# Kernel tuning notes

Hardware: AMD Instinct MI355X
Metric: run time of the kernel (lower is better)

Reference implementation:

```python
import jax, jax.numpy as jnp
import numpy as np

N = 24000; E = 384000; NT = 3; IN = 128; HID = 32; ED = 64; NE = 5; FFN = 64; C = 16
HEADS = (8, 8, 1); ALPHA = 0.05; DAL = 2


def _lrelu(x, s):
    return jnp.where(x >= 0, x, s * x)


def _elu(x):
    return jnp.where(x > 0, x, jnp.expm1(x))


def _ln(x, g, b, eps=1e-5):
    m = x.mean(-1, keepdims=True)
    v = ((x - m) ** 2).mean(-1, keepdims=True)
    return (x - m) / jnp.sqrt(v + eps) * g + b


def _l2n(x, eps=1e-12):
    return x / jnp.maximum(jnp.linalg.norm(x, axis=1, keepdims=True), eps)


def _ta(h, src, dst, e_feat, edge_emb, W, We, al, ar, ae, bias, res_W, res_attn, act):
    # SimpleHGN-style heterogeneous graph attention layer (TALayer)
    Hh = al.shape[0]
    feat = (h @ W).reshape(N, Hh, HID)                       # [N,H,D]
    ee = (edge_emb[e_feat] @ We).reshape(E, Hh, ED)          # [E,H,ED]
    el = (feat * al).sum(-1)                                 # [N,H]
    er = (feat * ar).sum(-1)                                 # [N,H]
    lg = _lrelu(el[src] + er[dst] + (ee * ae).sum(-1), 0.2)  # [E,H]
    m = jax.ops.segment_max(lg, dst, num_segments=N)         # edge softmax over dst
    a = jnp.exp(lg - m[dst])
    a = a / jax.ops.segment_sum(a, dst, num_segments=N)[dst]
    if res_attn is not None:
        a = a * (1.0 - ALPHA) + res_attn * ALPHA             # residual attention carry-over
    rst = jax.ops.segment_sum(a[:, :, None] * feat[src], dst, num_segments=N)
    if res_W is not None:
        rst = rst + (h @ res_W).reshape(N, Hh, HID)
    rst = rst + bias
    if act:
        rst = _elu(rst)
    return rst, jax.lax.stop_gradient(a)


def forward(feats, fc_W, fc_b, ntype_emb, W_ntype,
            ta0_edge_emb, ta0_W, ta0_We, ta0_al, ta0_ar, ta0_ae, ta0_bias,
            ta1_edge_emb, ta1_W, ta1_We, ta1_al, ta1_ar, ta1_ae, ta1_bias, ta1_res_W,
            ta2_edge_emb, ta2_W, ta2_We, ta2_al, ta2_ar, ta2_ae, ta2_bias, ta2_res_W,
            da_ln1_g, da_ln1_b, da_Wq, da_bq, da_Wk, da_bk, da_Wv, da_bv, da_Wo, da_bo,
            da_ln2_g, da_ln2_b, da_W1, da_b1, da_W2, da_b2, final_W, logits_W,
            e_feat, node_type, src, dst):
    # per-node-type input projection + leaky_relu(0.01), concat over types -> [N,HID]
    h = _lrelu(jnp.einsum('tni,tio->tno', feats, fc_W) + fc_b[:, None, :], 0.01).reshape(N, HID)
    ntype_feat = (ntype_emb @ W_ntype)[node_type]            # [N,HID]
    h = h * ntype_feat
    h0, a0 = _ta(h, src, dst, e_feat, ta0_edge_emb, ta0_W, ta0_We, ta0_al, ta0_ar, ta0_ae, ta0_bias, None, None, True)
    h = h0.reshape(N, -1)
    h1, _ = _ta(h, src, dst, e_feat, ta1_edge_emb, ta1_W, ta1_We, ta1_al, ta1_ar, ta1_ae, ta1_bias, ta1_res_W, a0, True)
    h = h1.reshape(N, -1)
    hf, _ = _ta(h, src, dst, e_feat, ta2_edge_emb, ta2_W, ta2_We, ta2_al, ta2_ar, ta2_ae, ta2_bias, ta2_res_W, None, False)
    h_feat = hf.reshape(N, HID)
    # dim-wise transformer (DALayer stack): tokens = HID dims, channel = 1
    x = (h_feat * ntype_feat)[:, :, None]                    # [N,HID,1]
    for l in range(DAL):
        y = _ln(x, da_ln1_g[l], da_ln1_b[l])
        q = y @ da_Wq[l] + da_bq[l]
        k = y @ da_Wk[l] + da_bk[l]
        v = y @ da_Wv[l] + da_bv[l]
        att = jax.nn.softmax(jnp.einsum('nqd,nkd->nqk', q, k), axis=-1)  # scale=att_size**-0.5=1
        x = x + (jnp.einsum('nqk,nkd->nqd', att, v) @ da_Wo[l] + da_bo[l])
        y = _ln(x, da_ln2_g[l], da_ln2_b[l])
        x = x + (jax.nn.gelu(y @ da_W1[l] + da_b1[l], approximate=False) @ da_W2[l] + da_b2[l])
    h_dim = _l2n(x[:, :, 0])
    h_final = jnp.concatenate([_l2n(h_feat), h_dim], axis=1) @ final_W
    logits = jax.nn.relu(h_final) @ logits_W
    return logits / jnp.maximum(jnp.linalg.norm(logits, axis=1, keepdims=True), 1e-12)


def setup_inputs():
    key = jax.random.key(0)
    ks = iter(jax.random.split(key, 96))
    def rn(shape, s=0.1):
        return jax.random.normal(next(ks), shape, jnp.float32) * s
    inp = {}
    inp["feats"] = jax.random.normal(next(ks), (NT, N // NT, IN), jnp.float32)
    inp["e_feat"] = jax.random.randint(next(ks), (E,), 0, NE)
    inp["node_type"] = jax.random.randint(next(ks), (N,), 0, NT)
    inp["src"] = jax.random.randint(next(ks), (E,), 0, N)
    inp["dst"] = jax.random.randint(next(ks), (E,), 0, N)
    inp["fc_W"] = rn((NT, IN, HID)); inp["fc_b"] = rn((NT, HID))
    inp["ntype_emb"] = rn((NT, HID)); inp["W_ntype"] = rn((HID, HID))
    ins = (HID, HID * HEADS[0], HID * HEADS[1])
    for l in range(3):
        Hh = HEADS[l]; di = ins[l]; p = "ta%d_" % l
        inp[p + "edge_emb"] = rn((NE, ED))
        inp[p + "W"] = rn((di, Hh * HID))
        inp[p + "We"] = rn((ED, Hh * ED))
        inp[p + "al"] = rn((Hh, HID)); inp[p + "ar"] = rn((Hh, HID)); inp[p + "ae"] = rn((Hh, ED))
        inp[p + "bias"] = jnp.zeros((Hh, HID), jnp.float32)
        if l > 0:
            inp[p + "res_W"] = rn((di, Hh * HID))
    inp["da_ln1_g"] = jnp.ones((DAL, 1), jnp.float32); inp["da_ln1_b"] = jnp.zeros((DAL, 1), jnp.float32)
    inp["da_Wq"] = rn((DAL, 1, 1)); inp["da_bq"] = jnp.zeros((DAL, 1), jnp.float32)
    inp["da_Wk"] = rn((DAL, 1, 1)); inp["da_bk"] = jnp.zeros((DAL, 1), jnp.float32)
    inp["da_Wv"] = rn((DAL, 1, 1)); inp["da_bv"] = jnp.zeros((DAL, 1), jnp.float32)
    inp["da_Wo"] = rn((DAL, 1, 1)); inp["da_bo"] = jnp.zeros((DAL, 1), jnp.float32)
    inp["da_ln2_g"] = jnp.ones((DAL, 1), jnp.float32); inp["da_ln2_b"] = jnp.zeros((DAL, 1), jnp.float32)
    inp["da_W1"] = rn((DAL, 1, FFN)); inp["da_b1"] = jnp.zeros((DAL, FFN), jnp.float32)
    inp["da_W2"] = rn((DAL, FFN, 1)); inp["da_b2"] = jnp.zeros((DAL, 1), jnp.float32)
    inp["final_W"] = rn((2 * HID, HID))
    inp["logits_W"] = rn((HID, C))
    return inp


def reference(feats, fc_W, fc_b, ntype_emb, W_ntype,
              ta0_edge_emb, ta0_W, ta0_We, ta0_al, ta0_ar, ta0_ae, ta0_bias,
              ta1_edge_emb, ta1_W, ta1_We, ta1_al, ta1_ar, ta1_ae, ta1_bias, ta1_res_W,
              ta2_edge_emb, ta2_W, ta2_We, ta2_al, ta2_ar, ta2_ae, ta2_bias, ta2_res_W,
              da_ln1_g, da_ln1_b, da_Wq, da_bq, da_Wk, da_bk, da_Wv, da_bv, da_Wo, da_bo,
              da_ln2_g, da_ln2_b, da_W1, da_b1, da_W2, da_b2, final_W, logits_W,
              e_feat, node_type, src, dst):
    return forward(feats, fc_W, fc_b, ntype_emb, W_ntype,
                   ta0_edge_emb, ta0_W, ta0_We, ta0_al, ta0_ar, ta0_ae, ta0_bias,
                   ta1_edge_emb, ta1_W, ta1_We, ta1_al, ta1_ar, ta1_ae, ta1_bias, ta1_res_W,
                   ta2_edge_emb, ta2_W, ta2_We, ta2_al, ta2_ar, ta2_ae, ta2_bias, ta2_res_W,
                   da_ln1_g, da_ln1_b, da_Wq, da_bq, da_Wk, da_bk, da_Wv, da_bv, da_Wo, da_bo,
                   da_ln2_g, da_ln2_b, da_W1, da_b1, da_W2, da_b2, final_W, logits_W,
                   e_feat, node_type, src, dst)
```

## Files before the change

### kernel.cpp

```cpp
#include <hip/hip_runtime.h>
#include <math.h>

constexpr int kN = 24000;
constexpr int kE = 384000;
constexpr float kAlpha = 0.05f;

typedef unsigned int   u32;
typedef unsigned short u16;
typedef __attribute__((ext_vector_type(8))) short short8;
typedef __attribute__((ext_vector_type(4))) float float4v;

__device__ __forceinline__ float bf2f(u16 x) { return __uint_as_float(((u32)x) << 16); }
__device__ __forceinline__ u16 f2bf(float f) {
  u32 u = __float_as_uint(f);
  return (u16)((u + 0x7fffu + ((u >> 16) & 1u)) >> 16);
}
__device__ __forceinline__ void bfrow32(const u16* __restrict__ p, float* f) {
  const uint4* q = (const uint4*)p;
  #pragma unroll
  for (int i = 0; i < 4; ++i) {
    uint4 w = q[i];
    f[i*8+0] = bf2f((u16)(w.x & 0xffff)); f[i*8+1] = bf2f((u16)(w.x >> 16));
    f[i*8+2] = bf2f((u16)(w.y & 0xffff)); f[i*8+3] = bf2f((u16)(w.y >> 16));
    f[i*8+4] = bf2f((u16)(w.z & 0xffff)); f[i*8+5] = bf2f((u16)(w.z >> 16));
    f[i*8+6] = bf2f((u16)(w.w & 0xffff)); f[i*8+7] = bf2f((u16)(w.w >> 16));
  }
}

__global__ void __launch_bounds__(256) zero_ints_kernel(int* __restrict__ p, int n) {
  int i = blockIdx.x * 256 + threadIdx.x;
  if (i < n) p[i] = 0;
}

__global__ void __launch_bounds__(256) count_kernel(const int* __restrict__ dst,
                                                    int* __restrict__ counts) {
  int e = blockIdx.x * 256 + threadIdx.x;
  if (e < kE) atomicAdd(&counts[dst[e]], 1);
}

__global__ void __launch_bounds__(1024) scan_kernel(const int* __restrict__ counts,
                                                    int* __restrict__ row_start) {
  __shared__ int wsum[16];
  __shared__ int carry_s;
  int tid = threadIdx.x, lane = tid & 63, wid = tid >> 6;
  if (tid == 0) { carry_s = 0; row_start[0] = 0; }
  __syncthreads();
  for (int base = 0; base < kN; base += 1024) {
    int x = (base + tid < kN) ? counts[base + tid] : 0;
    #pragma unroll
    for (int off = 1; off < 64; off <<= 1) {
      int y = __shfl_up(x, off);
      if (lane >= off) x += y;
    }
    if (lane == 63) wsum[wid] = x;
    __syncthreads();
    if (tid < 16) {
      int wv = wsum[tid];
      #pragma unroll
      for (int off = 1; off < 16; off <<= 1) {
        int y = __shfl_up(wv, off);
        if (tid >= off) wv += y;
      }
      wsum[tid] = wv;
    }
    __syncthreads();
    int incl = x + carry_s + (wid > 0 ? wsum[wid - 1] : 0);
    if (base + tid < kN) row_start[base + tid + 1] = incl;
    __syncthreads();
    if (tid == 1023) carry_s = incl;
    __syncthreads();
  }
}

__global__ void __launch_bounds__(256) scatter_kernel(const int* __restrict__ dst,
                                                      const int* __restrict__ row_start,
                                                      int* __restrict__ cursor,
                                                      int* __restrict__ edge_ids) {
  int e = blockIdx.x * 256 + threadIdx.x;
  if (e < kE) {
    int n = dst[e];
    int pos = row_start[n] + atomicAdd(&cursor[n], 1);
    edge_ids[pos] = e;
  }
}

__global__ void __launch_bounds__(1024) precompute_kernel(
    const float* __restrict__ ntype_emb, const float* __restrict__ W_ntype,
    const float* __restrict__ emb0, const float* __restrict__ We0, const float* __restrict__ ae0,
    const float* __restrict__ emb1, const float* __restrict__ We1, const float* __restrict__ ae1,
    const float* __restrict__ emb2, const float* __restrict__ We2, const float* __restrict__ ae2,
    const float* __restrict__ ln1_b, const float* __restrict__ Wv, const float* __restrict__ bv,
    const float* __restrict__ Wo, const float* __restrict__ bo,
    const float* __restrict__ ln2_b, const float* __restrict__ W1, const float* __restrict__ b1,
    const float* __restrict__ W2, const float* __restrict__ b2,
    float* __restrict__ ntf, float* __restrict__ eterm, float* __restrict__ dadelta) {
  __shared__ float wae[17][64];
  __shared__ float red[128];
  int tid = threadIdx.x;
  for (int idx = tid; idx < 17 * 64; idx += 1024) {
    int hg = idx >> 6, k = idx & 63;
    const float* We; const float* ae; int Hh, h;
    if (hg < 8)       { We = We0; ae = ae0; Hh = 8; h = hg; }
    else if (hg < 16) { We = We1; ae = ae1; Hh = 8; h = hg - 8; }
    else              { We = We2; ae = ae2; Hh = 1; h = 0; }
    float s = 0.f;
    for (int d = 0; d < 64; ++d) s += We[(size_t)k * Hh * 64 + h * 64 + d] * ae[h * 64 + d];
    wae[hg][k] = s;
  }
  __syncthreads();
  if (tid < 85) {
    int id = tid;
    const float* emb; int Hh, t, h, hg, base;
    if (id < 40)      { emb = emb0; Hh = 8; t = id / 8;  h = id % 8; hg = h;      base = 0;  }
    else if (id < 80) { int i = id - 40; emb = emb1; Hh = 8; t = i / 8; h = i % 8; hg = 8 + h; base = 40; }
    else              { int i = id - 80; emb = emb2; Hh = 1; t = i;    h = 0;     hg = 16;    base = 80; }
    float s = 0.f;
    for (int k = 0; k < 64; ++k) s += emb[t * 64 + k] * wae[hg][k];
    eterm[base + t * Hh + h] = s;
  } else if (tid >= 128 && tid < 224) {
    int idx = tid - 128;
    int t = idx / 32, o = idx % 32;
    float s = 0.f;
    for (int k = 0; k < 32; ++k) s += ntype_emb[t * 32 + k] * W_ntype[k * 32 + o];
    ntf[idx] = s;
  } else if (tid >= 256 && tid < 384) {
    int i2 = tid - 256;
    int l = i2 >> 6, j = i2 & 63;
    float u = ln2_b[l] * W1[l * 64 + j] + b1[l * 64 + j];
    float g = 0.5f * u * (1.0f + erff(u * 0.7071067811865476f));
    red[i2] = g * W2[l * 64 + j];
  }
  __syncthreads();
  if (tid == 0) {
    float delta = 0.f;
    for (int l = 0; l < 2; ++l) {
      float vs = ln1_b[l] * Wv[l] + bv[l];
      delta += vs * Wo[l] + bo[l] + b2[l];
    }
    for (int i = 0; i < 128; ++i) delta += red[i];
    *dadelta = delta;
  }
}

__global__ void __launch_bounds__(256) pack_kernel(
    const float* __restrict__ W0, const float* __restrict__ al0, const float* __restrict__ ar0,
    const float* __restrict__ W1, const float* __restrict__ al1, const float* __restrict__ ar1,
    const float* __restrict__ rW1,
    const float* __restrict__ W2, const float* __restrict__ al2, const float* __restrict__ ar2,
    const float* __restrict__ rW2,
    u16* __restrict__ WT0, u16* __restrict__ WT1, u16* __restrict__ WT2) {
  const int SZ0 = 320 * 32, SZ1 = 576 * 256;
  int tid = blockIdx.x * 256 + threadIdx.x;
  float v = 0.f;
  if (tid < SZ0) {
    int n = tid / 32, k = tid % 32;
    if (n < 256) v = W0[k * 256 + n];
    else if (n < 264) { int h = n - 256; for (int d = 0; d < 32; ++d) v += W0[k * 256 + h * 32 + d] * al0[h * 32 + d]; }
    else if (n < 272) { int h = n - 264; for (int d = 0; d < 32; ++d) v += W0[k * 256 + h * 32 + d] * ar0[h * 32 + d]; }
    WT0[n * 32 + k] = f2bf(v);
  } else if (tid < SZ0 + SZ1) {
    int i = tid - SZ0;
    int n = i / 256, k = i % 256;
    if (n < 256) v = W1[k * 256 + n];
    else if (n < 264) { int h = n - 256; for (int d = 0; d < 32; ++d) v += W1[k * 256 + h * 32 + d] * al1[h * 32 + d]; }
    else if (n < 272) { int h = n - 264; for (int d = 0; d < 32; ++d) v += W1[k * 256 + h * 32 + d] * ar1[h * 32 + d]; }
    else if (n < 528) v = rW1[k * 256 + (n - 272)];
    WT1[n * 256 + k] = f2bf(v);
  } else {
    int i = tid - SZ0 - SZ1;
    int n = i / 256, k = i % 256;
    if (n < 32) v = W2[k * 32 + n];
    else if (n == 32) { for (int d = 0; d < 32; ++d) v += W2[k * 32 + d] * al2[d]; }
    else if (n == 33) { for (int d = 0; d < 32; ++d) v += W2[k * 32 + d] * ar2[d]; }
    else if (n < 66) v = rW2[k * 32 + (n - 34)];
    WT2[n * 256 + k] = f2bf(v);
  }
}

__global__ void __launch_bounds__(256) inproj_kernel(
    const float* __restrict__ feats, const float* __restrict__ fc_W,
    const float* __restrict__ fc_b, const float* __restrict__ ntf,
    const int* __restrict__ node_type, u16* __restrict__ hb) {
  int t = blockIdx.x * 256 + threadIdx.x;
  if (t >= kN * 32) return;
  int n = t >> 5, o = t & 31;
  int ty = n / 8000;
  const float* fr = &feats[(size_t)n * 128];
  const float* w  = &fc_W[(size_t)ty * 4096 + o];
  float s = fc_b[ty * 32 + o];
  #pragma unroll
  for (int k = 0; k < 128; k += 4) {
    float4 f = *(const float4*)&fr[k];
    s += f.x * w[(k + 0) * 32] + f.y * w[(k + 1) * 32]
       + f.z * w[(k + 2) * 32] + f.w * w[(k + 3) * 32];
  }
  s = (s < 0.f) ? 0.01f * s : s;
  hb[t] = f2bf(s * ntf[node_type[n] * 32 + o]);
}

__global__ void __launch_bounds__(256) mfma_gemm_kernel(
    const u16* __restrict__ A, const u16* __restrict__ WT,
    const float* __restrict__ bias,
    u16* __restrict__ featb, float* __restrict__ el, float* __restrict__ er,
    u16* __restrict__ resb, float* __restrict__ resf,
    int K, int N1, int HH, int N2) {
  __shared__ __align__(16) u16 BsT[64 * 256];
  __shared__ __align__(16) u16 As[64 * 32];
  const int tid = threadIdx.x;
  const int l = tid & 63;
  const int w = tid >> 6;
  const int wm = w >> 1, wn = w & 1;
  const int m0 = blockIdx.y * 64;
  const int n0 = blockIdx.x * 64;
  const int kslot = l >> 4;
  const int l15 = l & 15;

  {
    const int cpr = K >> 3;
    const int total = 64 * cpr;
    for (int c = tid; c < total; c += 256) {
      int row = c / cpr, ch = c - row * cpr;
      uint4 v = *(const uint4*)(WT + (size_t)(n0 + row) * K + ch * 8);
      int off = ((row * K + ch * 8) * 2) ^ ((row & 7) << 4);
      *(uint4*)((char*)BsT + off) = v;
    }
  }

  float4v acc[2][2];
  #pragma unroll
  for (int f = 0; f < 2; ++f)
    #pragma unroll
    for (int g = 0; g < 2; ++g) { acc[f][g][0]=0.f; acc[f][g][1]=0.f; acc[f][g][2]=0.f; acc[f][g][3]=0.f; }

  for (int kc = 0; kc < K; kc += 32) {
    __syncthreads();
    {
      int row = tid >> 2, ks = tid & 3;
      uint4 v = *(const uint4*)(A + (size_t)(m0 + row) * K + kc + ks * 8);
      int off = (row * 64 + ks * 16) ^ ((row & 7) << 4);
      *(uint4*)((char*)As + off) = v;
    }
    __syncthreads();
    short8 af[2], bf[2];
    #pragma unroll
    for (int f = 0; f < 2; ++f) {
      int row = wm * 32 + f * 16 + l15;
      int off = (row * 64 + kslot * 16) ^ ((row & 7) << 4);
      af[f] = *(const short8*)((const char*)As + off);
    }
    #pragma unroll
    for (int g = 0; g < 2; ++g) {
      int n = wn * 32 + g * 16 + l15;
      int off = ((n * K + kc + kslot * 8) * 2) ^ ((n & 7) << 4);
      bf[g] = *(const short8*)((const char*)BsT + off);
    }
    #pragma unroll
    for (int f = 0; f < 2; ++f)
      #pragma unroll
      for (int g = 0; g < 2; ++g)
        acc[f][g] = __builtin_amdgcn_mfma_f32_16x16x32_bf16(af[f], bf[g], acc[f][g], 0, 0, 0);
  }

  const int rbase = kslot * 4;
  #pragma unroll
  for (int f = 0; f < 2; ++f) {
    #pragma unroll
    for (int g = 0; g < 2; ++g) {
      int gc = n0 + wn * 32 + g * 16 + l15;
      #pragma unroll
      for (int reg = 0; reg < 4; ++reg) {
        int gr = m0 + wm * 32 + f * 16 + rbase + reg;
        float v = acc[f][g][reg];
        if (gc < N1) {
          featb[(size_t)gr * N1 + gc] = f2bf(v);
        } else if (gc < N1 + HH) {
          el[(size_t)gr * HH + (gc - N1)] = v;
        } else if (gc < N1 + 2 * HH) {
          er[(size_t)gr * HH + (gc - N1 - HH)] = v;
        } else if (gc < N1 + 2 * HH + N2) {
          int c2 = gc - N1 - 2 * HH;
          float vv = v + bias[c2];
          if (resb) resb[(size_t)gr * N2 + c2] = f2bf(vv);
          else      resf[(size_t)gr * N2 + c2] = vv;
        }
      }
    }
  }
}

template <bool WRITE_A0, bool READ_A0, bool BIAS_INIT, bool ACT>
__global__ void __launch_bounds__(256) agg8w_kernel(
    const int* __restrict__ row_start, const int* __restrict__ edge_ids,
    const int* __restrict__ src, const int* __restrict__ ef,
    const float* __restrict__ el, const float* __restrict__ er,
    const float* __restrict__ eterm,
    const u16* __restrict__ featb,
    const float* __restrict__ bias,
    _Float16* __restrict__ a0h,
    const u16* __restrict__ accb,
    u16* __restrict__ outb) {
  int gw = (blockIdx.x * 256 + threadIdx.x) >> 6;
  if (gw >= kN) return;
  int l = threadIdx.x & 63;
  int h = l >> 3, s = l & 7;
  int s0 = row_start[gw], s1 = row_start[gw + 1];
  float ern = er[gw * 8 + h];
  float m = -1e30f, ssum = 0.f;
  for (int i = s0 + s; i < s1; i += 8) {
    int e = edge_ids[i];
    float lg = el[src[e] * 8 + h] + ern + eterm[ef[e] * 8 + h];
    lg = (lg < 0.f) ? 0.2f * lg : lg;
    if (lg > m) { ssum = ssum * expf(m - lg) + 1.f; m = lg; }
    else        { ssum += expf(lg - m); }
  }
  #pragma unroll
  for (int mk = 1; mk <= 4; mk <<= 1) {
    float om = __shfl_xor(m, mk);
    float os = __shfl_xor(ssum, mk);
    float nm = fmaxf(m, om);
    ssum = ssum * expf(m - nm) + os * expf(om - nm);
    m = nm;
  }
  float inv = 1.f / ssum;
  float4 acc;
  if (BIAS_INIT) {
    acc = *(const float4*)(bias + h * 32 + s * 4);
  } else {
    ushort4 rv = *(const ushort4*)(accb + (size_t)gw * 256 + l * 4);
    acc = make_float4(bf2f(rv.x), bf2f(rv.y), bf2f(rv.z), bf2f(rv.w));
  }
  for (int i = s0; i < s1; ++i) {
    int e = edge_ids[i];
    int se = src[e];
    float lg = el[se * 8 + h] + ern + eterm[ef[e] * 8 + h];
    lg = (lg < 0.f) ? 0.2f * lg : lg;
    float a = expf(lg - m) * inv;
    if (WRITE_A0) { if (s == 0) a0h[(size_t)e * 8 + h] = (_Float16)a; }
    if (READ_A0)  a = a * (1.f - kAlpha) + (float)a0h[(size_t)e * 8 + h] * kAlpha;
    ushort4 fv = *(const ushort4*)(featb + (size_t)se * 256 + l * 4);
    acc.x = fmaf(a, bf2f(fv.x), acc.x);
    acc.y = fmaf(a, bf2f(fv.y), acc.y);
    acc.z = fmaf(a, bf2f(fv.z), acc.z);
    acc.w = fmaf(a, bf2f(fv.w), acc.w);
  }
  if (ACT) {
    acc.x = (acc.x > 0.f) ? acc.x : expm1f(acc.x);
    acc.y = (acc.y > 0.f) ? acc.y : expm1f(acc.y);
    acc.z = (acc.z > 0.f) ? acc.z : expm1f(acc.z);
    acc.w = (acc.w > 0.f) ? acc.w : expm1f(acc.w);
  }
  ushort4 p;
  p.x = f2bf(acc.x); p.y = f2bf(acc.y); p.z = f2bf(acc.z); p.w = f2bf(acc.w);
  *(ushort4*)(outb + (size_t)gw * 256 + l * 4) = p;
}

__global__ void __launch_bounds__(256) agg1t_kernel(
    const int* __restrict__ row_start, const int* __restrict__ edge_ids,
    const int* __restrict__ src, const int* __restrict__ ef,
    const float* __restrict__ el, const float* __restrict__ er,
    const float* __restrict__ eterm,
    const u16* __restrict__ featb,
    float* __restrict__ rst) {
  int t = blockIdx.x * 256 + threadIdx.x;
  if (t >= kN) return;
  int s0 = row_start[t], s1 = row_start[t + 1];
  float ern = er[t];
  float acc[32];
  #pragma unroll
  for (int q = 0; q < 8; ++q) {
    float4 v = *(const float4*)&rst[(size_t)t * 32 + q * 4];
    acc[q*4] = v.x; acc[q*4+1] = v.y; acc[q*4+2] = v.z; acc[q*4+3] = v.w;
  }
  if (s0 < s1) {
    float m = -1e30f, ssum = 0.f;
    for (int i = s0; i < s1; ++i) {
      int e = edge_ids[i];
      float lg = el[src[e]] + ern + eterm[ef[e]];
      lg = (lg < 0.f) ? 0.2f * lg : lg;
      if (lg > m) { ssum = ssum * expf(m - lg) + 1.f; m = lg; }
      else        { ssum += expf(lg - m); }
    }
    float inv = 1.f / ssum;
    for (int i = s0; i < s1; ++i) {
      int e = edge_ids[i];
      int se = src[e];
      float lg = el[se] + ern + eterm[ef[e]];
      lg = (lg < 0.f) ? 0.2f * lg : lg;
      float a = expf(lg - m) * inv;
      float f[32];
      bfrow32(&featb[(size_t)se * 32], f);
      #pragma unroll
      for (int d = 0; d < 32; ++d) acc[d] = fmaf(a, f[d], acc[d]);
    }
  }
  #pragma unroll
  for (int q = 0; q < 8; ++q)
    *(float4*)&rst[(size_t)t * 32 + q * 4] =
        make_float4(acc[q*4], acc[q*4+1], acc[q*4+2], acc[q*4+3]);
}

__global__ void __launch_bounds__(256) final_kernel(
    const float* __restrict__ hfeat, const float* __restrict__ ntf,
    const int* __restrict__ node_type, const float* __restrict__ dadelta,
    const float* __restrict__ finalW, const float* __restrict__ logitsW,
    float* __restrict__ out) {
  int n = blockIdx.x * 256 + threadIdx.x;
  if (n >= kN) return;
  float delta = dadelta[0];
  const float* hf = &hfeat[(size_t)n * 32];
  const float* nt = &ntf[node_type[n] * 32];
  float a[32], b[32];
  float na = 0.f, nb = 0.f;
  #pragma unroll
  for (int d = 0; d < 32; ++d) {
    float x = hf[d];
    a[d] = x; na += x * x;
    float y = x * nt[d] + delta;
    b[d] = y; nb += y * y;
  }
  float inva = 1.f / fmaxf(sqrtf(na), 1e-12f);
  float invb = 1.f / fmaxf(sqrtf(nb), 1e-12f);
  #pragma unroll
  for (int d = 0; d < 32; ++d) { a[d] *= inva; b[d] *= invb; }
  float lg[16];
  #pragma unroll
  for (int c = 0; c < 16; ++c) lg[c] = 0.f;
  for (int o = 0; o < 32; ++o) {
    float s = 0.f;
    #pragma unroll
    for (int d = 0; d < 32; ++d)
      s += a[d] * finalW[d * 32 + o] + b[d] * finalW[(32 + d) * 32 + o];
    s = fmaxf(s, 0.f);
    #pragma unroll
    for (int c = 0; c < 16; ++c) lg[c] += s * logitsW[o * 16 + c];
  }
  float nl = 0.f;
  #pragma unroll
  for (int c = 0; c < 16; ++c) nl += lg[c] * lg[c];
  float invl = 1.f / fmaxf(sqrtf(nl), 1e-12f);
  #pragma unroll
  for (int c = 0; c < 16; ++c) out[(size_t)n * 16 + c] = lg[c] * invl;
}

extern "C" void kernel_launch(void* const* d_in, const int* in_sizes, int n_in,
                              void* d_out, int out_size, void* d_ws, size_t ws_size,
                              hipStream_t stream) {
  const float* feats     = (const float*)d_in[0];
  const int*   e_feat    = (const int*)d_in[1];
  const int*   node_type = (const int*)d_in[2];
  const int*   src       = (const int*)d_in[3];
  const int*   dst       = (const int*)d_in[4];
  const float* fc_W      = (const float*)d_in[5];
  const float* fc_b      = (const float*)d_in[6];
  const float* ntype_emb = (const float*)d_in[7];
  const float* W_ntype   = (const float*)d_in[8];
  const float* ta_edge_emb[3] = {(const float*)d_in[9],  (const float*)d_in[16], (const float*)d_in[24]};
  const float* ta_W[3]        = {(const float*)d_in[10], (const float*)d_in[17], (const float*)d_in[25]};
  const float* ta_We[3]       = {(const float*)d_in[11], (const float*)d_in[18], (const float*)d_in[26]};
  const float* ta_al[3]       = {(const float*)d_in[12], (const float*)d_in[19], (const float*)d_in[27]};
  const float* ta_ar[3]       = {(const float*)d_in[13], (const float*)d_in[20], (const float*)d_in[28]};
  const float* ta_ae[3]       = {(const float*)d_in[14], (const float*)d_in[21], (const float*)d_in[29]};
  const float* ta_bias[3]     = {(const float*)d_in[15], (const float*)d_in[22], (const float*)d_in[30]};
  const float* ta1_res_W = (const float*)d_in[23];
  const float* ta2_res_W = (const float*)d_in[31];
  const float* da_ln1_b  = (const float*)d_in[33];
  const float* da_Wv     = (const float*)d_in[38];
  const float* da_bv     = (const float*)d_in[39];
  const float* da_Wo     = (const float*)d_in[40];
  const float* da_bo     = (const float*)d_in[41];
  const float* da_ln2_b  = (const float*)d_in[43];
  const float* da_W1     = (const float*)d_in[44];
  const float* da_b1     = (const float*)d_in[45];
  const float* da_W2     = (const float*)d_in[46];
  const float* da_b2     = (const float*)d_in[47];
  const float* final_W   = (const float*)d_in[48];
  const float* logits_W  = (const float*)d_in[49];
  float* out = (float*)d_out;

  char* base = (char*)d_ws;
  int* iws       = (int*)base;
  int* counts    = iws;
  int* cursor    = iws + kN;
  int* row_start = iws + 2 * kN;
  int* edge_ids  = iws + 2 * kN + kN + 1;
  char* p = base + (size_t)456004 * 4;
  float* ntf = (float*)p;                     p += 512;
  float* etm = (float*)p;                     p += 512;
  float* dad = (float*)p;                     p += 64;
  float* el  = (float*)p;                     p += (size_t)kN * 8 * 4;
  float* er  = (float*)p;                     p += (size_t)kN * 8 * 4;
  float* S2  = (float*)p;                     p += (size_t)kN * 32 * 4;
  u16*   Hb  = (u16*)p;                       p += (size_t)kN * 32 * 2;
  _Float16* a0h = (_Float16*)p;               p += (size_t)kE * 8 * 2;
  u16* featb = (u16*)p;                       p += (size_t)kN * 256 * 2;
  u16* Rb0   = (u16*)p;                       p += (size_t)kN * 256 * 2;
  u16* Rpr   = (u16*)p;                       p += (size_t)kN * 256 * 2;
  u16* WT0   = (u16*)p;                       p += (size_t)320 * 32 * 2;
  u16* WT1   = (u16*)p;                       p += (size_t)576 * 256 * 2;
  u16* WT2   = (u16*)p;                       p += (size_t)128 * 256 * 2;

  zero_ints_kernel<<<(2 * kN + 255) / 256, 256, 0, stream>>>(counts, 2 * kN);
  count_kernel<<<kE / 256, 256, 0, stream>>>(dst, counts);
  scan_kernel<<<1, 1024, 0, stream>>>(counts, row_start);
  scatter_kernel<<<kE / 256, 256, 0, stream>>>(dst, row_start, cursor, edge_ids);

  precompute_kernel<<<1, 1024, 0, stream>>>(
      ntype_emb, W_ntype,
      ta_edge_emb[0], ta_We[0], ta_ae[0],
      ta_edge_emb[1], ta_We[1], ta_ae[1],
      ta_edge_emb[2], ta_We[2], ta_ae[2],
      da_ln1_b, da_Wv, da_bv, da_Wo, da_bo,
      da_ln2_b, da_W1, da_b1, da_W2, da_b2,
      ntf, etm, dad);
  pack_kernel<<<744, 256, 0, stream>>>(
      ta_W[0], ta_al[0], ta_ar[0],
      ta_W[1], ta_al[1], ta_ar[1], ta1_res_W,
      ta_W[2], ta_al[2], ta_ar[2], ta2_res_W,
      WT0, WT1, WT2);

  inproj_kernel<<<(kN * 32) / 256, 256, 0, stream>>>(feats, fc_W, fc_b, ntf, node_type, Hb);

  mfma_gemm_kernel<<<dim3(5, kN / 64), 256, 0, stream>>>(
      Hb, WT0, nullptr, featb, el, er, nullptr, nullptr, 32, 256, 8, 0);
  agg8w_kernel<true, false, true, true><<<kN / 4, 256, 0, stream>>>(
      row_start, edge_ids, src, e_feat, el, er, etm, featb, ta_bias[0], a0h, nullptr, Rb0);

  mfma_gemm_kernel<<<dim3(9, kN / 64), 256, 0, stream>>>(
      Rb0, WT1, ta_bias[1], featb, el, er, Rpr, nullptr, 256, 256, 8, 256);
  agg8w_kernel<false, true, false, true><<<kN / 4, 256, 0, stream>>>(
      row_start, edge_ids, src, e_feat, el, er, etm + 40, featb, nullptr, a0h, Rpr, Rpr);

  mfma_gemm_kernel<<<dim3(2, kN / 64), 256, 0, stream>>>(
      Rpr, WT2, ta_bias[2], featb, el, er, nullptr, S2, 256, 32, 1, 32);
  agg1t_kernel<<<(kN + 255) / 256, 256, 0, stream>>>(
      row_start, edge_ids, src, e_feat, el, er, etm + 80, featb, S2);

  final_kernel<<<(kN + 255) / 256, 256, 0, stream>>>(S2, ntf, node_type, dad, final_W, logits_W, out);
}
```

Measured before the change: 603.1 us.

## Fuse setup and final kernels, restructure GEMM staging and aggregation parallelism

Merges the precompute and pack kernels into one launch, and fuses the last-layer aggregation with the final projection kernel. The MFMA GEMM is templated on K and loads the whole A and B tiles into shared memory once, replacing the per-k-chunk sync loop. The 8-head aggregation now uses two waves per node with 16 lanes per head, caches edge-type terms in registers instead of gathering them, and prefetches edge indices ahead. Together these aim to cut launch overhead, synchronisation and gather latency, at the cost of more shared memory per GEMM block (64 KB when K=256), which may lower occupancy.

```diff
diff --git a/kernel.cpp b/kernel.cpp
--- a/kernel.cpp
+++ b/kernel.cpp
@@ -84,96 +84,95 @@
   }
 }
 
-__global__ void __launch_bounds__(1024) precompute_kernel(
+__global__ void __launch_bounds__(256) prepack_kernel(
+    const float* __restrict__ W0, const float* __restrict__ al0, const float* __restrict__ ar0,
+    const float* __restrict__ W1, const float* __restrict__ al1, const float* __restrict__ ar1,
+    const float* __restrict__ rW1,
+    const float* __restrict__ W2, const float* __restrict__ al2, const float* __restrict__ ar2,
+    const float* __restrict__ rW2,
+    u16* __restrict__ WT0, u16* __restrict__ WT1, u16* __restrict__ WT2,
     const float* __restrict__ ntype_emb, const float* __restrict__ W_ntype,
     const float* __restrict__ emb0, const float* __restrict__ We0, const float* __restrict__ ae0,
     const float* __restrict__ emb1, const float* __restrict__ We1, const float* __restrict__ ae1,
     const float* __restrict__ emb2, const float* __restrict__ We2, const float* __restrict__ ae2,
     const float* __restrict__ ln1_b, const float* __restrict__ Wv, const float* __restrict__ bv,
     const float* __restrict__ Wo, const float* __restrict__ bo,
-    const float* __restrict__ ln2_b, const float* __restrict__ W1, const float* __restrict__ b1,
-    const float* __restrict__ W2, const float* __restrict__ b2,
+    const float* __restrict__ ln2_b, const float* __restrict__ DW1, const float* __restrict__ Db1,
+    const float* __restrict__ DW2, const float* __restrict__ Db2,
     float* __restrict__ ntf, float* __restrict__ eterm, float* __restrict__ dadelta) {
   __shared__ float wae[17][64];
   __shared__ float red[128];
   int tid = threadIdx.x;
-  for (int idx = tid; idx < 17 * 64; idx += 1024) {
-    int hg = idx >> 6, k = idx & 63;
-    const float* We; const float* ae; int Hh, h;
-    if (hg < 8)       { We = We0; ae = ae0; Hh = 8; h = hg; }
-    else if (hg < 16) { We = We1; ae = ae1; Hh = 8; h = hg - 8; }
-    else              { We = We2; ae = ae2; Hh = 1; h = 0; }
-    float s = 0.f;
-    for (int d = 0; d < 64; ++d) s += We[(size_t)k * Hh * 64 + h * 64 + d] * ae[h * 64 + d];
-    wae[hg][k] = s;
-  }
-  __syncthreads();
-  if (tid < 85) {
-    int id = tid;
-    const float* emb; int Hh, t, h, hg, base;
-    if (id < 40)      { emb = emb0; Hh = 8; t = id / 8;  h = id % 8; hg = h;      base = 0;  }
-    else if (id < 80) { int i = id - 40; emb = emb1; Hh = 8; t = i / 8; h = i % 8; hg = 8 + h; base = 40; }
-    else              { int i = id - 80; emb = emb2; Hh = 1; t = i;    h = 0;     hg = 16;    base = 80; }
-    float s = 0.f;
-    for (int k = 0; k < 64; ++k) s += emb[t * 64 + k] * wae[hg][k];
-    eterm[base + t * Hh + h] = s;
-  } else if (tid >= 128 && tid < 224) {
-    int idx = tid - 128;
-    int t = idx / 32, o = idx % 32;
-    float s = 0.f;
-    for (int k = 0; k < 32; ++k) s += ntype_emb[t * 32 + k] * W_ntype[k * 32 + o];
-    ntf[idx] = s;
-  } else if (tid >= 256 && tid < 384) {
-    int i2 = tid - 256;
-    int l = i2 >> 6, j = i2 & 63;
-    float u = ln2_b[l] * W1[l * 64 + j] + b1[l * 64 + j];
-    float g = 0.5f * u * (1.0f + erff(u * 0.7071067811865476f));
-    red[i2] = g * W2[l * 64 + j];
-  }
-  __syncthreads();
-  if (tid == 0) {
-    float delta = 0.f;
-    for (int l = 0; l < 2; ++l) {
-      float vs = ln1_b[l] * Wv[l] + bv[l];
-      delta += vs * Wo[l] + bo[l] + b2[l];
-    }
-    for (int i = 0; i < 128; ++i) delta += red[i];
-    *dadelta = delta;
-  }
-}
-
-__global__ void __launch_bounds__(256) pack_kernel(
-    const float* __restrict__ W0, const float* __restrict__ al0, const float* __restrict__ ar0,
-    const float* __restrict__ W1, const float* __restrict__ al1, const float* __restrict__ ar1,
-    const float* __restrict__ rW1,
-    const float* __restrict__ W2, const float* __restrict__ al2, const float* __restrict__ ar2,
-    const float* __restrict__ rW2,
-    u16* __restrict__ WT0, u16* __restrict__ WT1, u16* __restrict__ WT2) {
-  const int SZ0 = 320 * 32, SZ1 = 576 * 256;
-  int tid = blockIdx.x * 256 + threadIdx.x;
-  float v = 0.f;
-  if (tid < SZ0) {
-    int n = tid / 32, k = tid % 32;
-    if (n < 256) v = W0[k * 256 + n];
-    else if (n < 264) { int h = n - 256; for (int d = 0; d < 32; ++d) v += W0[k * 256 + h * 32 + d] * al0[h * 32 + d]; }
-    else if (n < 272) { int h = n - 264; for (int d = 0; d < 32; ++d) v += W0[k * 256 + h * 32 + d] * ar0[h * 32 + d]; }
-    WT0[n * 32 + k] = f2bf(v);
-  } else if (tid < SZ0 + SZ1) {
-    int i = tid - SZ0;
-    int n = i / 256, k = i % 256;
-    if (n < 256) v = W1[k * 256 + n];
-    else if (n < 264) { int h = n - 256; for (int d = 0; d < 32; ++d) v += W1[k * 256 + h * 32 + d] * al1[h * 32 + d]; }
-    else if (n < 272) { int h = n - 264; for (int d = 0; d < 32; ++d) v += W1[k * 256 + h * 32 + d] * ar1[h * 32 + d]; }
-    else if (n < 528) v = rW1[k * 256 + (n - 272)];
-    WT1[n * 256 + k] = f2bf(v);
+  if (blockIdx.x < 744) {
+    const int SZ0 = 320 * 32, SZ1 = 576 * 256;
+    int gid = blockIdx.x * 256 + tid;
+    float v = 0.f;
+    if (gid < SZ0) {
+      int n = gid / 32, k = gid % 32;
+      if (n < 256) v = W0[k * 256 + n];
+      else if (n < 264) { int h = n - 256; for (int d = 0; d < 32; ++d) v += W0[k * 256 + h * 32 + d] * al0[h * 32 + d]; }
+      else if (n < 272) { int h = n - 264; for (int d = 0; d < 32; ++d) v += W0[k * 256 + h * 32 + d] * ar0[h * 32 + d]; }
+      WT0[n * 32 + k] = f2bf(v);
+    } else if (gid < SZ0 + SZ1) {
+      int i = gid - SZ0;
+      int n = i / 256, k = i % 256;
+      if (n < 256) v = W1[k * 256 + n];
+      else if (n < 264) { int h = n - 256; for (int d = 0; d < 32; ++d) v += W1[k * 256 + h * 32 + d] * al1[h * 32 + d]; }
+      else if (n < 272) { int h = n - 264; for (int d = 0; d < 32; ++d) v += W1[k * 256 + h * 32 + d] * ar1[h * 32 + d]; }
+      else if (n < 528) v = rW1[k * 256 + (n - 272)];
+      WT1[n * 256 + k] = f2bf(v);
+    } else {
+      int i = gid - SZ0 - SZ1;
+      int n = i / 256, k = i % 256;
+      if (n < 32) v = W2[k * 32 + n];
+      else if (n == 32) { for (int d = 0; d < 32; ++d) v += W2[k * 32 + d] * al2[d]; }
+      else if (n == 33) { for (int d = 0; d < 32; ++d) v += W2[k * 32 + d] * ar2[d]; }
+      else if (n < 66) v = rW2[k * 32 + (n - 34)];
+      WT2[n * 256 + k] = f2bf(v);
+    }
   } else {
-    int i = tid - SZ0 - SZ1;
-    int n = i / 256, k = i % 256;
-    if (n < 32) v = W2[k * 32 + n];
-    else if (n == 32) { for (int d = 0; d < 32; ++d) v += W2[k * 32 + d] * al2[d]; }
-    else if (n == 33) { for (int d = 0; d < 32; ++d) v += W2[k * 32 + d] * ar2[d]; }
-    else if (n < 66) v = rW2[k * 32 + (n - 34)];
-    WT2[n * 256 + k] = f2bf(v);
+    for (int idx = tid; idx < 17 * 64; idx += 256) {
+      int hg = idx >> 6, k = idx & 63;
+      const float* We; const float* ae; int Hh, h;
+      if (hg < 8)       { We = We0; ae = ae0; Hh = 8; h = hg; }
+      else if (hg < 16) { We = We1; ae = ae1; Hh = 8; h = hg - 8; }
+      else              { We = We2; ae = ae2; Hh = 1; h = 0; }
+      float s = 0.f;
+      for (int d = 0; d < 64; ++d) s += We[(size_t)k * Hh * 64 + h * 64 + d] * ae[h * 64 + d];
+      wae[hg][k] = s;
+    }
+    __syncthreads();
+    for (int id = tid; id < 85; id += 256) {
+      const float* emb; int Hh, t, h, hg, base;
+      if (id < 40)      { emb = emb0; Hh = 8; t = id / 8;  h = id % 8; hg = h;      base = 0;  }
+      else if (id < 80) { int i = id - 40; emb = emb1; Hh = 8; t = i / 8; h = i % 8; hg = 8 + h; base = 40; }
+      else              { int i = id - 80; emb = emb2; Hh = 1; t = i;    h = 0;     hg = 16;    base = 80; }
+      float s = 0.f;
+      for (int k = 0; k < 64; ++k) s += emb[t * 64 + k] * wae[hg][k];
+      eterm[base + t * Hh + h] = s;
+    }
+    for (int idx = tid; idx < 96; idx += 256) {
+      int t = idx / 32, o = idx % 32;
+      float s = 0.f;
+      for (int k = 0; k < 32; ++k) s += ntype_emb[t * 32 + k] * W_ntype[k * 32 + o];
+      ntf[idx] = s;
+    }
+    for (int i2 = tid; i2 < 128; i2 += 256) {
+      int l = i2 >> 6, j = i2 & 63;
+      float u = ln2_b[l] * DW1[l * 64 + j] + Db1[l * 64 + j];
+      float g = 0.5f * u * (1.0f + erff(u * 0.7071067811865476f));
+      red[i2] = g * DW2[l * 64 + j];
+    }
+    __syncthreads();
+    if (tid == 0) {
+      float delta = 0.f;
+      for (int l = 0; l < 2; ++l) {
+        float vs = ln1_b[l] * Wv[l] + bv[l];
+        delta += vs * Wo[l] + bo[l] + Db2[l];
+      }
+      for (int i = 0; i < 128; ++i) delta += red[i];
+      *dadelta = delta;
+    }
   }
 }
 
@@ -198,14 +197,17 @@
   hb[t] = f2bf(s * ntf[node_type[n] * 32 + o]);
 }
 
+template <int K>
 __global__ void __launch_bounds__(256) mfma_gemm_kernel(
     const u16* __restrict__ A, const u16* __restrict__ WT,
     const float* __restrict__ bias,
     u16* __restrict__ featb, float* __restrict__ el, float* __restrict__ er,
     u16* __restrict__ resb, float* __restrict__ resf,
-    int K, int N1, int HH, int N2) {
-  __shared__ __align__(16) u16 BsT[64 * 256];
-  __shared__ __align__(16) u16 As[64 * 32];
+    int N1, int HH, int N2) {
+  constexpr int RB = K * 2;
+  constexpr int CPR = K / 8;
+  __shared__ __align__(16) u16 As[64 * K];
+  __shared__ __align__(16) u16 Bs[64 * K];
   const int tid = threadIdx.x;
   const int l = tid & 63;
   const int w = tid >> 6;
@@ -215,16 +217,16 @@
   const int kslot = l >> 4;
   const int l15 = l & 15;
 
-  {
-    const int cpr = K >> 3;
-    const int total = 64 * cpr;
-    for (int c = tid; c < total; c += 256) {
-      int row = c / cpr, ch = c - row * cpr;
-      uint4 v = *(const uint4*)(WT + (size_t)(n0 + row) * K + ch * 8);
-      int off = ((row * K + ch * 8) * 2) ^ ((row & 7) << 4);
-      *(uint4*)((char*)BsT + off) = v;
-    }
-  }
+  #pragma unroll
+  for (int c = tid; c < 64 * CPR; c += 256) {
+    int row = c / CPR, ch = c - row * CPR;
+    int off = (row * RB + ch * 16) ^ ((row & 7) << 4);
+    uint4 va = *(const uint4*)(A + (size_t)(m0 + row) * K + ch * 8);
+    *(uint4*)((char*)As + off) = va;
+    uint4 vb = *(const uint4*)(WT + (size_t)(n0 + row) * K + ch * 8);
+    *(uint4*)((char*)Bs + off) = vb;
+  }
+  __syncthreads();
 
   float4v acc[2][2];
   #pragma unroll
@@ -232,27 +234,20 @@
     #pragma unroll
     for (int g = 0; g < 2; ++g) { acc[f][g][0]=0.f; acc[f][g][1]=0.f; acc[f][g][2]=0.f; acc[f][g][3]=0.f; }
 
+  #pragma unroll
   for (int kc = 0; kc < K; kc += 32) {
-    __syncthreads();
-    {
-      int row = tid >> 2, ks = tid & 3;
-      uint4 v = *(const uint4*)(A + (size_t)(m0 + row) * K + kc + ks * 8);
-      int off = (row * 64 + ks * 16) ^ ((row & 7) << 4);
-      *(uint4*)((char*)As + off) = v;
-    }
-    __syncthreads();
     short8 af[2], bf[2];
     #pragma unroll
     for (int f = 0; f < 2; ++f) {
       int row = wm * 32 + f * 16 + l15;
-      int off = (row * 64 + kslot * 16) ^ ((row & 7) << 4);
+      int off = (row * RB + kc * 2 + kslot * 16) ^ ((row & 7) << 4);
       af[f] = *(const short8*)((const char*)As + off);
     }
     #pragma unroll
     for (int g = 0; g < 2; ++g) {
       int n = wn * 32 + g * 16 + l15;
-      int off = ((n * K + kc + kslot * 8) * 2) ^ ((n & 7) << 4);
-      bf[g] = *(const short8*)((const char*)BsT + off);
+      int off = (n * RB + kc * 2 + kslot * 16) ^ ((n & 7) << 4);
+      bf[g] = *(const short8*)((const char*)Bs + off);
     }
     #pragma unroll
     for (int f = 0; f < 2; ++f)
@@ -300,21 +295,27 @@
     const u16* __restrict__ accb,
     u16* __restrict__ outb) {
   int gw = (blockIdx.x * 256 + threadIdx.x) >> 6;
-  if (gw >= kN) return;
+  if (gw >= kN * 2) return;
+  int n = gw >> 1, half = gw & 1;
   int l = threadIdx.x & 63;
-  int h = l >> 3, s = l & 7;
-  int s0 = row_start[gw], s1 = row_start[gw + 1];
-  float ern = er[gw * 8 + h];
+  int h = half * 4 + (l >> 4);
+  int q = l & 15;
+  int s0 = row_start[n], s1 = row_start[n + 1];
+  float ern = er[n * 8 + h];
+  float et0 = eterm[0 * 8 + h], et1 = eterm[1 * 8 + h], et2 = eterm[2 * 8 + h];
+  float et3 = eterm[3 * 8 + h], et4 = eterm[4 * 8 + h];
   float m = -1e30f, ssum = 0.f;
-  for (int i = s0 + s; i < s1; i += 8) {
+  for (int i = s0 + q; i < s1; i += 16) {
     int e = edge_ids[i];
-    float lg = el[src[e] * 8 + h] + ern + eterm[ef[e] * 8 + h];
+    int efc = ef[e];
+    float etv = (efc == 0) ? et0 : (efc == 1) ? et1 : (efc == 2) ? et2 : (efc == 3) ? et3 : et4;
+    float lg = el[src[e] * 8 + h] + ern + etv;
     lg = (lg < 0.f) ? 0.2f * lg : lg;
     if (lg > m) { ssum = ssum * expf(m - lg) + 1.f; m = lg; }
     else        { ssum += expf(lg - m); }
   }
   #pragma unroll
-  for (int mk = 1; mk <= 4; mk <<= 1) {
+  for (int mk = 1; mk <= 8; mk <<= 1) {
     float om = __shfl_xor(m, mk);
     float os = __shfl_xor(ssum, mk);
     float nm = fmaxf(m, om);
@@ -322,69 +323,81 @@
     m = nm;
   }
   float inv = 1.f / ssum;
-  float4 acc;
+  float ax, ay;
+  const size_t rowoff = (size_t)n * 256 + h * 32 + q * 2;
   if (BIAS_INIT) {
-    acc = *(const float4*)(bias + h * 32 + s * 4);
+    ax = bias[h * 32 + q * 2]; ay = bias[h * 32 + q * 2 + 1];
   } else {
-    ushort4 rv = *(const ushort4*)(accb + (size_t)gw * 256 + l * 4);
-    acc = make_float4(bf2f(rv.x), bf2f(rv.y), bf2f(rv.z), bf2f(rv.w));
-  }
+    u32 rv = *(const u32*)(accb + rowoff);
+    ax = bf2f((u16)(rv & 0xffff)); ay = bf2f((u16)(rv >> 16));
+  }
+  int e0 = 0, se0 = 0, ef0 = 0, e1 = 0, se1 = 0, ef1 = 0;
+  if (s0 < s1)     { e0 = edge_ids[s0];     se0 = src[e0]; ef0 = ef[e0]; }
+  if (s0 + 1 < s1) { e1 = edge_ids[s0 + 1]; se1 = src[e1]; ef1 = ef[e1]; }
   for (int i = s0; i < s1; ++i) {
-    int e = edge_ids[i];
-    int se = src[e];
-    float lg = el[se * 8 + h] + ern + eterm[ef[e] * 8 + h];
+    int e = e0, se = se0, efc = ef0;
+    e0 = e1; se0 = se1; ef0 = ef1;
+    if (i + 2 < s1) { e1 = edge_ids[i + 2]; se1 = src[e1]; ef1 = ef[e1]; }
+    float elv = el[se * 8 + h];
+    u32 fv = *(const u32*)(featb + (size_t)se * 256 + h * 32 + q * 2);
+    float etv = (efc == 0) ? et0 : (efc == 1) ? et1 : (efc == 2) ? et2 : (efc == 3) ? et3 : et4;
+    float lg = elv + ern + etv;
     lg = (lg < 0.f) ? 0.2f * lg : lg;
     float a = expf(lg - m) * inv;
-    if (WRITE_A0) { if (s == 0) a0h[(size_t)e * 8 + h] = (_Float16)a; }
+    if (WRITE_A0) { if (q == 0) a0h[(size_t)e * 8 + h] = (_Float16)a; }
     if (READ_A0)  a = a * (1.f - kAlpha) + (float)a0h[(size_t)e * 8 + h] * kAlpha;
-    ushort4 fv = *(const ushort4*)(featb + (size_t)se * 256 + l * 4);
-    acc.x = fmaf(a, bf2f(fv.x), acc.x);
-    acc.y = fmaf(a, bf2f(fv.y), acc.y);
-    acc.z = fmaf(a, bf2f(fv.z), acc.z);
-    acc.w = fmaf(a, bf2f(fv.w), acc.w);
+    ax = fmaf(a, bf2f((u16)(fv & 0xffff)), ax);
+    ay = fmaf(a, bf2f((u16)(fv >> 16)), ay);
   }
   if (ACT) {
-    acc.x = (acc.x > 0.f) ? acc.x : expm1f(acc.x);
-    acc.y = (acc.y > 0.f) ? acc.y : expm1f(acc.y);
-    acc.z = (acc.z > 0.f) ? acc.z : expm1f(acc.z);
-    acc.w = (acc.w > 0.f) ? acc.w : expm1f(acc.w);
-  }
-  ushort4 p;
-  p.x = f2bf(acc.x); p.y = f2bf(acc.y); p.z = f2bf(acc.z); p.w = f2bf(acc.w);
-  *(ushort4*)(outb + (size_t)gw * 256 + l * 4) = p;
-}
-
-__global__ void __launch_bounds__(256) agg1t_kernel(
+    ax = (ax > 0.f) ? ax : expm1f(ax);
+    ay = (ay > 0.f) ? ay : expm1f(ay);
+  }
+  u32 pw = (u32)f2bf(ax) | ((u32)f2bf(ay) << 16);
+  *(u32*)(outb + rowoff) = pw;
+}
+
+__global__ void __launch_bounds__(256) agg1t_final_kernel(
     const int* __restrict__ row_start, const int* __restrict__ edge_ids,
     const int* __restrict__ src, const int* __restrict__ ef,
     const float* __restrict__ el, const float* __restrict__ er,
     const float* __restrict__ eterm,
     const u16* __restrict__ featb,
-    float* __restrict__ rst) {
-  int t = blockIdx.x * 256 + threadIdx.x;
-  if (t >= kN) return;
-  int s0 = row_start[t], s1 = row_start[t + 1];
-  float ern = er[t];
+    const float* __restrict__ S2,
+    const float* __restrict__ ntf, const int* __restrict__ node_type,
+    const float* __restrict__ dadelta,
+    const float* __restrict__ finalW, const float* __restrict__ logitsW,
+    float* __restrict__ out) {
+  int n = blockIdx.x * 256 + threadIdx.x;
+  if (n >= kN) return;
+  int s0 = row_start[n], s1 = row_start[n + 1];
+  float ern = er[n];
+  float et0 = eterm[0], et1 = eterm[1], et2 = eterm[2], et3 = eterm[3], et4 = eterm[4];
   float acc[32];
   #pragma unroll
-  for (int q = 0; q < 8; ++q) {
-    float4 v = *(const float4*)&rst[(size_t)t * 32 + q * 4];
-    acc[q*4] = v.x; acc[q*4+1] = v.y; acc[q*4+2] = v.z; acc[q*4+3] = v.w;
+  for (int d2 = 0; d2 < 8; ++d2) {
+    float4 v = *(const float4*)&S2[(size_t)n * 32 + d2 * 4];
+    acc[d2*4] = v.x; acc[d2*4+1] = v.y; acc[d2*4+2] = v.z; acc[d2*4+3] = v.w;
   }
   if (s0 < s1) {
     float m = -1e30f, ssum = 0.f;
     for (int i = s0; i < s1; ++i) {
       int e = edge_ids[i];
-      float lg = el[src[e]] + ern + eterm[ef[e]];
+      int efc = ef[e];
+      float etv = (efc == 0) ? et0 : (efc == 1) ? et1 : (efc == 2) ? et2 : (efc == 3) ? et3 : et4;
+      float lg = el[src[e]] + ern + etv;
       lg = (lg < 0.f) ? 0.2f * lg : lg;
       if (lg > m) { ssum = ssum * expf(m - lg) + 1.f; m = lg; }
       else        { ssum += expf(lg - m); }
     }
     float inv = 1.f / ssum;
+    int e0 = 0, se0 = 0, ef0 = 0;
+    e0 = edge_ids[s0]; se0 = src[e0]; ef0 = ef[e0];
     for (int i = s0; i < s1; ++i) {
-      int e = edge_ids[i];
-      int se = src[e];
-      float lg = el[se] + ern + eterm[ef[e]];
+      int e = e0, se = se0, efc = ef0;
+      if (i + 1 < s1) { e0 = edge_ids[i + 1]; se0 = src[e0]; ef0 = ef[e0]; }
+      float etv = (efc == 0) ? et0 : (efc == 1) ? et1 : (efc == 2) ? et2 : (efc == 3) ? et3 : et4;
+      float lg = el[se] + ern + etv;
       lg = (lg < 0.f) ? 0.2f * lg : lg;
       float a = expf(lg - m) * inv;
       float f[32];
@@ -393,35 +406,21 @@
       for (int d = 0; d < 32; ++d) acc[d] = fmaf(a, f[d], acc[d]);
     }
   }
-  #pragma unroll
-  for (int q = 0; q < 8; ++q)
-    *(float4*)&rst[(size_t)t * 32 + q * 4] =
-        make_float4(acc[q*4], acc[q*4+1], acc[q*4+2], acc[q*4+3]);
-}
-
-__global__ void __launch_bounds__(256) final_kernel(
-    const float* __restrict__ hfeat, const float* __restrict__ ntf,
-    const int* __restrict__ node_type, const float* __restrict__ dadelta,
-    const float* __restrict__ finalW, const float* __restrict__ logitsW,
-    float* __restrict__ out) {
-  int n = blockIdx.x * 256 + threadIdx.x;
-  if (n >= kN) return;
   float delta = dadelta[0];
-  const float* hf = &hfeat[(size_t)n * 32];
   const float* nt = &ntf[node_type[n] * 32];
-  float a[32], b[32];
+  float a_[32], b_[32];
   float na = 0.f, nb = 0.f;
   #pragma unroll
   for (int d = 0; d < 32; ++d) {
-    float x = hf[d];
-    a[d] = x; na += x * x;
+    float x = acc[d];
+    a_[d] = x; na += x * x;
     float y = x * nt[d] + delta;
-    b[d] = y; nb += y * y;
+    b_[d] = y; nb += y * y;
   }
   float inva = 1.f / fmaxf(sqrtf(na), 1e-12f);
   float invb = 1.f / fmaxf(sqrtf(nb), 1e-12f);
   #pragma unroll
-  for (int d = 0; d < 32; ++d) { a[d] *= inva; b[d] *= invb; }
+  for (int d = 0; d < 32; ++d) { a_[d] *= inva; b_[d] *= invb; }
   float lg[16];
   #pragma unroll
   for (int c = 0; c < 16; ++c) lg[c] = 0.f;
@@ -429,7 +428,7 @@
     float s = 0.f;
     #pragma unroll
     for (int d = 0; d < 32; ++d)
-      s += a[d] * finalW[d * 32 + o] + b[d] * finalW[(32 + d) * 32 + o];
+      s += a_[d] * finalW[d * 32 + o] + b_[d] * finalW[(32 + d) * 32 + o];
     s = fmaxf(s, 0.f);
     #pragma unroll
     for (int c = 0; c < 16; ++c) lg[c] += s * logitsW[o * 16 + c];
@@ -504,7 +503,11 @@
   scan_kernel<<<1, 1024, 0, stream>>>(counts, row_start);
   scatter_kernel<<<kE / 256, 256, 0, stream>>>(dst, row_start, cursor, edge_ids);
 
-  precompute_kernel<<<1, 1024, 0, stream>>>(
+  prepack_kernel<<<745, 256, 0, stream>>>(
+      ta_W[0], ta_al[0], ta_ar[0],
+      ta_W[1], ta_al[1], ta_ar[1], ta1_res_W,
+      ta_W[2], ta_al[2], ta_ar[2], ta2_res_W,
+      WT0, WT1, WT2,
       ntype_emb, W_ntype,
       ta_edge_emb[0], ta_We[0], ta_ae[0],
       ta_edge_emb[1], ta_We[1], ta_ae[1],
@@ -512,28 +515,22 @@
       da_ln1_b, da_Wv, da_bv, da_Wo, da_bo,
       da_ln2_b, da_W1, da_b1, da_W2, da_b2,
       ntf, etm, dad);
-  pack_kernel<<<744, 256, 0, stream>>>(
-      ta_W[0], ta_al[0], ta_ar[0],
-      ta_W[1], ta_al[1], ta_ar[1], ta1_res_W,
-      ta_W[2], ta_al[2], ta_ar[2], ta2_res_W,
-      WT0, WT1, WT2);
 
   inproj_kernel<<<(kN * 32) / 256, 256, 0, stream>>>(feats, fc_W, fc_b, ntf, node_type, Hb);
 
-  mfma_gemm_kernel<<<dim3(5, kN / 64), 256, 0, stream>>>(
-      Hb, WT0, nullptr, featb, el, er, nullptr, nullptr, 32, 256, 8, 0);
-  agg8w_kernel<true, false, true, true><<<kN / 4, 256, 0, stream>>>(
+  mfma_gemm_kernel<32><<<dim3(5, kN / 64), 256, 0, stream>>>(
+      Hb, WT0, nullptr, featb, el, er, nullptr, nullptr, 256, 8, 0);
+  agg8w_kernel<true, false, true, true><<<kN / 2, 256, 0, stream>>>(
       row_start, edge_ids, src, e_feat, el, er, etm, featb, ta_bias[0], a0h, nullptr, Rb0);
 
-  mfma_gemm_kernel<<<dim3(9, kN / 64), 256, 0, stream>>>(
-      Rb0, WT1, ta_bias[1], featb, el, er, Rpr, nullptr, 256, 256, 8, 256);
-  agg8w_kernel<false, true, false, true><<<kN / 4, 256, 0, stream>>>(
+  mfma_gemm_kernel<256><<<dim3(9, kN / 64), 256, 0, stream>>>(
+      Rb0, WT1, ta_bias[1], featb, el, er, Rpr, nullptr, 256, 8, 256);
+  agg8w_kernel<false, true, false, true><<<kN / 2, 256, 0, stream>>>(
       row_start, edge_ids, src, e_feat, el, er, etm + 40, featb, nullptr, a0h, Rpr, Rpr);
 
-  mfma_gemm_kernel<<<dim3(2, kN / 64), 256, 0, stream>>>(
-      Rpr, WT2, ta_bias[2], featb, el, er, nullptr, S2, 256, 32, 1, 32);
-  agg1t_kernel<<<(kN + 255) / 256, 256, 0, stream>>>(
-      row_start, edge_ids, src, e_feat, el, er, etm + 80, featb, S2);
-
-  final_kernel<<<(kN + 255) / 256, 256, 0, stream>>>(S2, ntf, node_type, dad, final_W, logits_W, out);
-}
+  mfma_gemm_kernel<256><<<dim3(2, kN / 64), 256, 0, stream>>>(
+      Rpr, WT2, ta_bias[2], featb, el, er, nullptr, S2, 32, 1, 32);
+  agg1t_final_kernel<<<(kN + 255) / 256, 256, 0, stream>>>(
+      row_start, edge_ids, src, e_feat, el, er, etm + 80, featb, S2,
+      ntf, node_type, dad, final_W, logits_W, out);
+}
```

After: 662.1 us. 9.8% more time.
